# Kernel optimization log

Hardware: AMD Instinct MI355X
Metric: run time of the kernel (lower is better)

The kernel has to match this reference:

```python
import jax, jax.numpy as jnp
import numpy as np

U_UNITS = 256

def _lstm(x, mask, W, U, b, reverse):
    # x: [B,T,F], mask: [B,T] bool (True = valid). Keras semantics: masked steps
    # carry state and previous output through unchanged.
    B = x.shape[0]
    u = U.shape[0]
    xW = jnp.einsum('btf,fg->btg', x, W) + b  # precompute input projection
    def step(carry, inp):
        h, c = carry
        xw, m = inp
        z = xw + h @ U
        i, f, g, o = jnp.split(z, 4, axis=-1)
        i = jax.nn.sigmoid(i)
        f = jax.nn.sigmoid(f)
        g = jnp.tanh(g)
        o = jax.nn.sigmoid(o)
        cn = f * c + i * g
        hn = o * jnp.tanh(cn)
        m2 = m[:, None]
        hn = jnp.where(m2, hn, h)
        cn = jnp.where(m2, cn, c)
        return (hn, cn), hn
    init = (jnp.zeros((B, u), x.dtype), jnp.zeros((B, u), x.dtype))
    xs = (jnp.swapaxes(xW, 0, 1), jnp.swapaxes(mask, 0, 1))
    _, hs = jax.lax.scan(step, init, xs, reverse=reverse)
    return jnp.swapaxes(hs, 0, 1)

def _bilstm(x, mask, Wf, Uf, bf, Wb, Ub, bb):
    hf = _lstm(x, mask, Wf, Uf, bf, False)
    hb = _lstm(x, mask, Wb, Ub, bb, True)
    return jnp.concatenate([hf, hb], axis=-1)

def setup_inputs():
    key = jax.random.key(0)
    B, T, F, U = 32, 2048, 64, U_UNITS
    H = 2 * U
    ks = jax.random.split(key, 40)
    def gl(k, shape):
        return (jax.random.normal(k, shape, jnp.float32) / np.sqrt(shape[0])).astype(jnp.float32)
    d = {}
    d['x'] = jax.random.normal(ks[0], (B, T, F), jnp.float32)
    d['x_mask'] = jax.random.randint(ks[1], (B, T), 0, 2, jnp.int32)
    d['training'] = 0
    # layer 0: input F; layer 1: input 2U
    d['Wf0'] = gl(ks[2], (F, 4 * U)); d['Uf0'] = gl(ks[3], (U, 4 * U)); d['bf0'] = jnp.zeros((4 * U,), jnp.float32)
    d['Wb0'] = gl(ks[4], (F, 4 * U)); d['Ub0'] = gl(ks[5], (U, 4 * U)); d['bb0'] = jnp.zeros((4 * U,), jnp.float32)
    d['Wf1'] = gl(ks[6], (H, 4 * U)); d['Uf1'] = gl(ks[7], (U, 4 * U)); d['bf1'] = jnp.zeros((4 * U,), jnp.float32)
    d['Wb1'] = gl(ks[8], (H, 4 * U)); d['Ub1'] = gl(ks[9], (U, 4 * U)); d['bb1'] = jnp.zeros((4 * U,), jnp.float32)
    # output heads
    d['Wp'] = gl(ks[10], (H, 2)); d['bp'] = jnp.zeros((2,), jnp.float32)
    d['Wbu'] = gl(ks[11], (H, 2)); d['bbu'] = jnp.zeros((2,), jnp.float32)
    d['W3'] = gl(ks[12], (H, 3)); d['b3'] = jnp.zeros((3,), jnp.float32)
    d['W8'] = gl(ks[13], (H, 8)); d['b8'] = jnp.zeros((8,), jnp.float32)
    d['Wa'] = gl(ks[14], (H, 1)); d['ba'] = jnp.zeros((1,), jnp.float32)
    d['Wpp'] = gl(ks[15], (H, 4)); d['bpp'] = jnp.zeros((4,), jnp.float32)
    return d

def reference(x, x_mask, training, Wf0, Uf0, bf0, Wb0, Ub0, bb0, Wf1, Uf1, bf1, Wb1, Ub1, bb1, Wp, bp, Wbu, bbu, W3, b3, W8, b8, Wa, ba, Wpp, bpp):
    mask = x_mask != 1  # tf.logical_not(tf.equal(x_mask, 1))
    h = _bilstm(x, mask, Wf0, Uf0, bf0, Wb0, Ub0, bb0)
    h = _bilstm(h, mask, Wf1, Uf1, bf1, Wb1, Ub1, bb1)
    h = jax.nn.relu(h)
    # dropout is identity at inference (training=0)
    ppi = jax.nn.softmax(h @ Wp + bp, axis=-1)
    buried = h @ Wbu + bbu
    ss3 = h @ W3 + b3
    ss8 = h @ W8 + b8
    asa = h @ Wa + ba
    phipsi = h @ Wpp + bpp
    return (ppi, buried, ss3, ss8, asa, phipsi)
```

## Files before the change

kernel.cpp:

```cpp
#include <hip/hip_runtime.h>
#include <stdint.h>


#define T_SEQ 2048
#define BATCH 32
#define NROWS 65536
#define NG 1024
#define FLG_STRIDE 32

typedef __attribute__((ext_vector_type(8))) short short8;
typedef __attribute__((ext_vector_type(4))) float f32x4;
typedef __attribute__((ext_vector_type(2))) float f32x2;

__device__ __forceinline__ ushort f32_to_bf16(float f) {
    uint32_t u = __float_as_uint(f);
    u = u + 0x7FFFu + ((u >> 16) & 1u);
    return (ushort)(u >> 16);
}
__device__ __forceinline__ float bf16_to_f32(ushort h) {
    return __uint_as_float(((uint32_t)h) << 16);
}
__device__ __forceinline__ uint64_t split_pack4(f32x4 v, uint64_t& lo64) {
    ushort h0 = f32_to_bf16(v[0]), h1 = f32_to_bf16(v[1]);
    ushort h2 = f32_to_bf16(v[2]), h3 = f32_to_bf16(v[3]);
    ushort l0 = f32_to_bf16(v[0] - bf16_to_f32(h0));
    ushort l1 = f32_to_bf16(v[1] - bf16_to_f32(h1));
    ushort l2 = f32_to_bf16(v[2] - bf16_to_f32(h2));
    ushort l3 = f32_to_bf16(v[3] - bf16_to_f32(h3));
    lo64 = (uint64_t)l0 | ((uint64_t)l1 << 16) | ((uint64_t)l2 << 32) | ((uint64_t)l3 << 48);
    return (uint64_t)h0 | ((uint64_t)h1 << 16) | ((uint64_t)h2 << 32) | ((uint64_t)h3 << 48);
}

__global__ void init_ctrl_kernel(int* __restrict__ flags, int nf,
                                 unsigned long long* __restrict__ hxp, int nh) {
    int i = blockIdx.x * 256 + threadIdx.x;
    if (i < nf) flags[i] = 0;
    if (i < nh) hxp[i] = 0ull;
}

__global__ __launch_bounds__(256) void gemm_split_kernel(
    const float* __restrict__ A, int K,
    const float* __restrict__ Bw, const float* __restrict__ bias,
    float* __restrict__ Cc, int cb, int lsS, int dir)
{
    __shared__ __align__(16) ushort Ash[128 * 36];
    __shared__ __align__(16) ushort Asl[128 * 36];
    __shared__ __align__(16) ushort Bsh[128 * 36];
    __shared__ __align__(16) ushort Bsl[128 * 36];
    const int Smask = (1 << lsS) - 1;
    int t = threadIdx.x;
    int n0 = blockIdx.x * 128;
    int m0 = blockIdx.y * 128;
    int lane = t & 63, wv = t >> 6;
    int wr = wv >> 1, wc = wv & 1;
    int fr = lane & 15, fq = lane >> 4;

    f32x4 acc[4][4];
#pragma unroll
    for (int i = 0; i < 4; i++)
#pragma unroll
        for (int j = 0; j < 4; j++) acc[i][j] = (f32x4)(0.0f);

    int arow = t >> 1, ahalf = t & 1;
    int bc = t & 127, bkh = t >> 7;

    int loc_all = m0 + arow;
    int b = loc_all >> lsS;
    int loc = loc_all & Smask;
    int row_g = b * T_SEQ + (dir ? (T_SEQ - 1 - cb - loc) : (cb + loc));

    for (int k0 = 0; k0 < K; k0 += 32) {
        {
            const float* s = A + (size_t)row_g * K + k0 + ahalf * 16;
            uint64_t* dh = (uint64_t*)&Ash[arow * 36 + ahalf * 16];
            uint64_t* dl = (uint64_t*)&Asl[arow * 36 + ahalf * 16];
#pragma unroll
            for (int g = 0; g < 4; g++) {
                f32x4 v = ((const f32x4*)s)[g];
                uint64_t lo64;
                uint64_t hi64 = split_pack4(v, lo64);
                dh[g] = hi64; dl[g] = lo64;
            }
        }
        {
            float bv[16];
#pragma unroll
            for (int i = 0; i < 16; i++)
                bv[i] = Bw[(size_t)(k0 + bkh * 16 + i) * NG + n0 + bc];
            uint64_t* dh = (uint64_t*)&Bsh[bc * 36 + bkh * 16];
            uint64_t* dl = (uint64_t*)&Bsl[bc * 36 + bkh * 16];
#pragma unroll
            for (int g = 0; g < 4; g++) {
                f32x4 v = { bv[4 * g], bv[4 * g + 1], bv[4 * g + 2], bv[4 * g + 3] };
                uint64_t lo64;
                uint64_t hi64 = split_pack4(v, lo64);
                dh[g] = hi64; dl[g] = lo64;
            }
        }
        __syncthreads();
        union FU { uint64_t u[2]; short8 v; };
        FU bh[4], bl[4];
#pragma unroll
        for (int n = 0; n < 4; n++) {
            int boff = (wc * 64 + n * 16 + fr) * 36 + fq * 8;
            bh[n].u[0] = ((const uint64_t*)&Bsh[boff])[0];
            bh[n].u[1] = ((const uint64_t*)&Bsh[boff])[1];
            bl[n].u[0] = ((const uint64_t*)&Bsl[boff])[0];
            bl[n].u[1] = ((const uint64_t*)&Bsl[boff])[1];
        }
#pragma unroll
        for (int m = 0; m < 4; m++) {
            int aoff = (wr * 64 + m * 16 + fr) * 36 + fq * 8;
            FU ah, al;
            ah.u[0] = ((const uint64_t*)&Ash[aoff])[0];
            ah.u[1] = ((const uint64_t*)&Ash[aoff])[1];
            al.u[0] = ((const uint64_t*)&Asl[aoff])[0];
            al.u[1] = ((const uint64_t*)&Asl[aoff])[1];
#pragma unroll
            for (int n = 0; n < 4; n++) {
                acc[m][n] = __builtin_amdgcn_mfma_f32_16x16x32_bf16(ah.v, bh[n].v, acc[m][n], 0, 0, 0);
                acc[m][n] = __builtin_amdgcn_mfma_f32_16x16x32_bf16(ah.v, bl[n].v, acc[m][n], 0, 0, 0);
                acc[m][n] = __builtin_amdgcn_mfma_f32_16x16x32_bf16(al.v, bh[n].v, acc[m][n], 0, 0, 0);
            }
        }
        __syncthreads();
    }
#pragma unroll
    for (int m = 0; m < 4; m++)
#pragma unroll
        for (int n = 0; n < 4; n++) {
            int gcol = n0 + wc * 64 + n * 16 + fr;
            float bvv = bias[gcol];
#pragma unroll
            for (int i = 0; i < 4; i++) {
                int crow = m0 + wr * 64 + m * 16 + fq * 4 + i;
                Cc[(size_t)crow * NG + gcol] = acc[m][n][i] + bvv;
            }
        }
}

__global__ __launch_bounds__(512, 2) void lstm_kernel(
    const float* __restrict__ Uf, const float* __restrict__ Ub,
    const float* __restrict__ xWcf, const float* __restrict__ xWcb,
    const int* __restrict__ mask,
    float* __restrict__ houtF,
    ushort* __restrict__ houtB,
    unsigned long long* __restrict__ hxp,
    float* __restrict__ cstate,
    int* __restrict__ flags,
    int cb, int S)
{
    int wg = blockIdx.x;
    int chain = wg & 63;
    int w = wg >> 6;
    int dir = chain >> 5;
    int b = chain & 31;
    const float* U = dir ? Ub : Uf;
    const float* xWc = dir ? xWcb : xWcf;

    int t = threadIdx.x;
    __shared__ __align__(16) float hbuf[256];
    __shared__ __align__(16) float pbuf[4 * 256];
    __shared__ int mbuf[2048];

    int kchunk = t >> 7;
    int cg = t & 127;
    int q = cg >> 5;
    int jj0 = 2 * (cg & 31);
    int col0 = q * 256 + w * 64 + jj0;

    f32x2 Ur[64];
    {
        const float* Up = U + (size_t)(kchunk * 64) * NG + col0;
#pragma unroll
        for (int i = 0; i < 64; i++) Ur[i] = *(const f32x2*)(Up + (size_t)i * NG);
    }
    unsigned long long* hxpc = hxp + chain * 512;
    int* flg = flags + chain * FLG_STRIDE;
    int j = t & 63;
    int gj = w * 64 + j;
    int owner = t >> 6;

    for (int nl = t; nl < S; nl += 512) {
        int tp = dir ? (T_SEQ - 1 - (cb + nl)) : (cb + nl);
        mbuf[nl] = mask[b * T_SEQ + tp];
    }
    int kc = __hip_atomic_load(&flg[0], __ATOMIC_RELAXED, __HIP_MEMORY_SCOPE_AGENT);
    if (t < 256) {
        if (kc > 0) {
            unsigned long long pk = __hip_atomic_load(&hxpc[((kc - 1) & 1) * 256 + t],
                                                      __ATOMIC_RELAXED, __HIP_MEMORY_SCOPE_AGENT);
            hbuf[t] = __uint_as_float((uint32_t)pk);
        } else {
            hbuf[t] = 0.0f;
        }
    }
    float creg = 0.0f, hreg = 0.0f;
    if (t < 64) {
        if (cb != 0) creg = cstate[chain * 256 + gj];
        if (kc > 0) {
            unsigned long long pk = __hip_atomic_load(&hxpc[((kc - 1) & 1) * 256 + gj],
                                                      __ATOMIC_RELAXED, __HIP_MEMORY_SCOPE_AGENT);
            hreg = __uint_as_float((uint32_t)pk);
        }
    }
    __syncthreads();

    for (int nl = 0; nl < S; nl++) {
        int tp = dir ? (T_SEQ - 1 - (cb + nl)) : (cb + nl);
        size_t row_g = (size_t)b * T_SEQ + tp;
        int mval = mbuf[nl];
        if (mval == 1) {
            if (t < 64) {
                size_t oidx = row_g * 512 + dir * 256 + gj;
                if (houtF) houtF[oidx] = hreg;
                else       houtB[oidx] = f32_to_bf16(hreg);
            }
            continue;
        }
        float xw0 = 0.f, xw1 = 0.f, xw2 = 0.f, xw3 = 0.f;
        if (t < 64) {
            const float* xr = xWc + ((size_t)b * S + nl) * NG;
            xw0 = xr[gj];
            xw1 = xr[256 + gj];
            xw2 = xr[512 + gj];
            xw3 = xr[768 + gj];
        }
        if (kc > 0 && t < 256 && owner != w) {
            unsigned long long pk;
            for (;;) {
                pk = __hip_atomic_load(&hxpc[((kc - 1) & 1) * 256 + t],
                                       __ATOMIC_RELAXED, __HIP_MEMORY_SCOPE_AGENT);
                if ((uint32_t)(pk >> 32) >= (uint32_t)kc) break;
                __builtin_amdgcn_s_sleep(1);
            }
            hbuf[t] = __uint_as_float((uint32_t)pk);
        }
        __syncthreads();
        float a0 = 0.0f, a1 = 0.0f;
        {
            const float* hb = &hbuf[kchunk * 64];
#pragma unroll
            for (int i = 0; i < 16; i++) {
                f32x4 h4 = *(const f32x4*)(hb + 4 * i);
#pragma unroll
                for (int j2 = 0; j2 < 4; j2++) {
                    a0 += h4[j2] * Ur[4 * i + j2][0];
                    a1 += h4[j2] * Ur[4 * i + j2][1];
                }
            }
        }
        {
            f32x2 pv = {a0, a1};
            *(f32x2*)&pbuf[kchunk * 256 + 2 * cg] = pv;
        }
        __syncthreads();
        if (t < 64) {
            float zi = xw0 + pbuf[j]       + pbuf[256 + j]       + pbuf[512 + j]       + pbuf[768 + j];
            float zf = xw1 + pbuf[64 + j]  + pbuf[256 + 64 + j]  + pbuf[512 + 64 + j]  + pbuf[768 + 64 + j];
            float zg = xw2 + pbuf[128 + j] + pbuf[256 + 128 + j] + pbuf[512 + 128 + j] + pbuf[768 + 128 + j];
            float zo = xw3 + pbuf[192 + j] + pbuf[256 + 192 + j] + pbuf[512 + 192 + j] + pbuf[768 + 192 + j];
            float ig = 1.0f / (1.0f + expf(-zi));
            float fg = 1.0f / (1.0f + expf(-zf));
            float gg = tanhf(zg);
            float og = 1.0f / (1.0f + expf(-zo));
            float cn = fg * creg + ig * gg;
            float hn = og * tanhf(cn);
            creg = cn; hreg = hn;
            hbuf[gj] = hn;
            unsigned long long pk = ((unsigned long long)(uint32_t)(kc + 1) << 32)
                                  | (unsigned long long)(uint32_t)__float_as_uint(hn);
            __hip_atomic_store(&hxpc[(kc & 1) * 256 + gj], pk,
                               __ATOMIC_RELAXED, __HIP_MEMORY_SCOPE_AGENT);
            size_t oidx = row_g * 512 + dir * 256 + gj;
            if (houtF) houtF[oidx] = hn;
            else       houtB[oidx] = f32_to_bf16(hn);
        }
        kc++;
    }
    if (t < 64) cstate[chain * 256 + gj] = creg;
    if (w == 0 && t == 0)
        __hip_atomic_store(&flg[0], kc, __ATOMIC_RELAXED, __HIP_MEMORY_SCOPE_AGENT);
}

__global__ __launch_bounds__(256, 2) void heads_kernel(
    const ushort* __restrict__ h1,
    const float* __restrict__ Wp, const float* __restrict__ bp,
    const float* __restrict__ Wbu, const float* __restrict__ bbu,
    const float* __restrict__ W3, const float* __restrict__ b3,
    const float* __restrict__ W8, const float* __restrict__ b8,
    const float* __restrict__ Wa, const float* __restrict__ ba,
    const float* __restrict__ Wpp, const float* __restrict__ bpp,
    float* __restrict__ out)
{
    int gwv = (blockIdx.x * 256 + threadIdx.x) >> 6;
    int nwv = (gridDim.x * 256) >> 6;
    int lane = threadIdx.x & 63;
    int k0 = lane * 8;

    float wr_[8][20];
#pragma unroll
    for (int u = 0; u < 8; u++) {
        int k = k0 + u;
        wr_[u][0]  = Wp[k * 2];      wr_[u][1]  = Wp[k * 2 + 1];
        wr_[u][2]  = Wbu[k * 2];     wr_[u][3]  = Wbu[k * 2 + 1];
        wr_[u][4]  = W3[k * 3];      wr_[u][5]  = W3[k * 3 + 1];  wr_[u][6] = W3[k * 3 + 2];
#pragma unroll
        for (int c = 0; c < 8; c++) wr_[u][7 + c] = W8[k * 8 + c];
        wr_[u][15] = Wa[k];
#pragma unroll
        for (int c = 0; c < 4; c++) wr_[u][16 + c] = Wpp[k * 4 + c];
    }
    float myb = 0.0f;
    size_t ooff = 0;
    if (lane < 2)        { myb = bp[lane];        ooff = 0 + lane; }
    else if (lane < 4)   { myb = bbu[lane - 2];   ooff = (size_t)NROWS * 2 + (lane - 2); }
    else if (lane < 7)   { myb = b3[lane - 4];    ooff = (size_t)NROWS * 4 + (lane - 4); }
    else if (lane < 15)  { myb = b8[lane - 7];    ooff = (size_t)NROWS * 7 + (lane - 7); }
    else if (lane < 16)  { myb = ba[0];           ooff = (size_t)NROWS * 15; }
    else if (lane < 20)  { myb = bpp[lane - 16];  ooff = (size_t)NROWS * 16 + (lane - 16); }
    float bp0 = bp[0], bp1 = bp[1];
    int stride = (lane < 2) ? 2 : (lane < 4) ? 2 : (lane < 7) ? 3 : (lane < 15) ? 8 : (lane < 16) ? 1 : 4;

    for (int r = gwv; r < NROWS; r += nwv) {
        union { uint4 u4; ushort us[8]; } hu;
        hu.u4 = *(const uint4*)(h1 + (size_t)r * 512 + k0);
        float acc[20];
#pragma unroll
        for (int c = 0; c < 20; c++) acc[c] = 0.0f;
#pragma unroll
        for (int u = 0; u < 8; u++) {
            float hv = fmaxf(bf16_to_f32(hu.us[u]), 0.0f);
#pragma unroll
            for (int c = 0; c < 20; c++) acc[c] += hv * wr_[u][c];
        }
#pragma unroll
        for (int off = 32; off >= 1; off >>= 1)
#pragma unroll
            for (int c = 0; c < 20; c++) acc[c] += __shfl_xor(acc[c], off);
        if (lane < 20) {
            float v = acc[lane] + myb;
            if (lane < 2) {
                float s0 = acc[0] + bp0, s1 = acc[1] + bp1;
                float mx = fmaxf(s0, s1);
                float e0 = expf(s0 - mx), e1 = expf(s1 - mx);
                v = ((lane == 0) ? e0 : e1) / (e0 + e1);
            }
            out[ooff + (size_t)r * stride] = v;
        }
    }
}

extern "C" void kernel_launch(void* const* d_in, const int* in_sizes, int n_in,
                              void* d_out, int out_size, void* d_ws, size_t ws_size,
                              hipStream_t stream) {
    const float* x    = (const float*)d_in[0];
    const int* xmask  = (const int*)d_in[1];
    const float* Wf0  = (const float*)d_in[3];
    const float* Uf0  = (const float*)d_in[4];
    const float* bf0  = (const float*)d_in[5];
    const float* Wb0  = (const float*)d_in[6];
    const float* Ub0  = (const float*)d_in[7];
    const float* bb0  = (const float*)d_in[8];
    const float* Wf1  = (const float*)d_in[9];
    const float* Uf1  = (const float*)d_in[10];
    const float* bf1  = (const float*)d_in[11];
    const float* Wb1  = (const float*)d_in[12];
    const float* Ub1  = (const float*)d_in[13];
    const float* bb1  = (const float*)d_in[14];
    const float* Wp   = (const float*)d_in[15]; const float* bp  = (const float*)d_in[16];
    const float* Wbu  = (const float*)d_in[17]; const float* bbu = (const float*)d_in[18];
    const float* W3   = (const float*)d_in[19]; const float* b3  = (const float*)d_in[20];
    const float* W8   = (const float*)d_in[21]; const float* b8  = (const float*)d_in[22];
    const float* Wa   = (const float*)d_in[23]; const float* ba  = (const float*)d_in[24];
    const float* Wpp  = (const float*)d_in[25]; const float* bpp = (const float*)d_in[26];
    float* out = (float*)d_out;

    char* ws = (char*)d_ws;
    size_t off = 0;
    auto take = [&](size_t bytes) -> void* {
        void* p = ws + off;
        off += (bytes + 255) & ~(size_t)255;
        return p;
    };
    int* flags = (int*)take((size_t)2 * 64 * FLG_STRIDE * 4);
    unsigned long long* hxp = (unsigned long long*)take((size_t)2 * 64 * 2 * 256 * 8);
    float*  cstate = (float*)take((size_t)64 * 256 * 4);
    float*  h0F    = (float*)take((size_t)NROWS * 512 * 4);
    ushort* h1B    = (ushort*)take((size_t)NROWS * 512 * 2);
    size_t fixed = off;

    int S = 8, lsS = 3;
    for (int cand = 11; cand >= 3; cand--) {
        if (fixed + (((size_t)1 << cand) * 262144) + 4096 <= ws_size) { S = 1 << cand; lsS = cand; break; }
    }
    float* xWcf = (float*)take((size_t)BATCH * S * NG * 4);
    float* xWcb = (float*)take((size_t)BATCH * S * NG * 4);
    int NC = T_SEQ / S;
    (void)in_sizes; (void)n_in; (void)out_size;

    int nf = 2 * 64 * FLG_STRIDE;
    int nh = 2 * 64 * 2 * 256;
    int ninit = nh > nf ? nh : nf;
    init_ctrl_kernel<<<(ninit + 255) / 256, 256, 0, stream>>>(flags, nf, hxp, nh);

    dim3 ggrid(NG / 128, (BATCH * S) / 128);
    for (int c = 0; c < NC; c++) {
        int cb = c * S;
        gemm_split_kernel<<<ggrid, 256, 0, stream>>>(x, 64, Wf0, bf0, xWcf, cb, lsS, 0);
        gemm_split_kernel<<<ggrid, 256, 0, stream>>>(x, 64, Wb0, bb0, xWcb, cb, lsS, 1);
        lstm_kernel<<<256, 512, 0, stream>>>(Uf0, Ub0, xWcf, xWcb, xmask, h0F, nullptr,
                                             hxp, cstate, flags, cb, S);
    }
    for (int c = 0; c < NC; c++) {
        int cb = c * S;
        gemm_split_kernel<<<ggrid, 256, 0, stream>>>(h0F, 512, Wf1, bf1, xWcf, cb, lsS, 0);
        gemm_split_kernel<<<ggrid, 256, 0, stream>>>(h0F, 512, Wb1, bb1, xWcb, cb, lsS, 1);
        lstm_kernel<<<256, 512, 0, stream>>>(Uf1, Ub1, xWcf, xWcb, xmask, nullptr, h1B,
                                             hxp + (size_t)64 * 512, cstate, flags + 64 * FLG_STRIDE, cb, S);
    }

    heads_kernel<<<2048, 256, 0, stream>>>(
        h1B, Wp, bp, Wbu, bbu, W3, b3, W8, b8, Wa, ba, Wpp, bpp, out);
}
```

Measured before the change: 5.613 ms.

## Run each LSTM chain in one workgroup with fp16-packed recurrent weights and dot2

```diff
diff --git a/kernel.cpp b/kernel.cpp
--- a/kernel.cpp
+++ b/kernel.cpp
@@ -6,11 +6,11 @@
 #define BATCH 32
 #define NROWS 65536
 #define NG 1024
-#define FLG_STRIDE 32
 
 typedef __attribute__((ext_vector_type(8))) short short8;
 typedef __attribute__((ext_vector_type(4))) float f32x4;
 typedef __attribute__((ext_vector_type(2))) float f32x2;
+typedef _Float16 f16x2 __attribute__((ext_vector_type(2)));
 
 __device__ __forceinline__ ushort f32_to_bf16(float f) {
     uint32_t u = __float_as_uint(f);
@@ -30,12 +30,19 @@
     lo64 = (uint64_t)l0 | ((uint64_t)l1 << 16) | ((uint64_t)l2 << 32) | ((uint64_t)l3 << 48);
     return (uint64_t)h0 | ((uint64_t)h1 << 16) | ((uint64_t)h2 << 32) | ((uint64_t)h3 << 48);
 }
-
-__global__ void init_ctrl_kernel(int* __restrict__ flags, int nf,
-                                 unsigned long long* __restrict__ hxp, int nh) {
+__device__ __forceinline__ float fdot2_(uint32_t u, uint32_t h, float acc) {
+    asm("v_dot2_f32_f16 %0, %1, %2, %0" : "+v"(acc) : "v"(u), "v"(h));
+    return acc;
+}
+
+__global__ void upack_kernel(const float* __restrict__ U, uint32_t* __restrict__ Upk) {
     int i = blockIdx.x * 256 + threadIdx.x;
-    if (i < nf) flags[i] = 0;
-    if (i < nh) hxp[i] = 0ull;
+    if (i >= 128 * 1024) return;
+    int kp = i >> 10, col = i & 1023;
+    f16x2 v;
+    v[0] = (_Float16)U[(size_t)(2 * kp) * NG + col];
+    v[1] = (_Float16)U[(size_t)(2 * kp + 1) * NG + col];
+    Upk[i] = __builtin_bit_cast(uint32_t, v);
 }
 
 __global__ __launch_bounds__(256) void gemm_split_kernel(
@@ -140,126 +147,111 @@
 }
 
 __global__ __launch_bounds__(512, 2) void lstm_kernel(
-    const float* __restrict__ Uf, const float* __restrict__ Ub,
+    const uint32_t* __restrict__ Upkf, const uint32_t* __restrict__ Upkb,
     const float* __restrict__ xWcf, const float* __restrict__ xWcb,
     const int* __restrict__ mask,
     float* __restrict__ houtF,
-    ushort* __restrict__ houtB,
-    unsigned long long* __restrict__ hxp,
+    ushort* __restrict__ houtH,
+    float* __restrict__ hstate,
     float* __restrict__ cstate,
-    int* __restrict__ flags,
     int cb, int S)
 {
-    int wg = blockIdx.x;
-    int chain = wg & 63;
-    int w = wg >> 6;
+    int chain = blockIdx.x;
     int dir = chain >> 5;
     int b = chain & 31;
-    const float* U = dir ? Ub : Uf;
+    const uint32_t* Upk = dir ? Upkb : Upkf;
     const float* xWc = dir ? xWcb : xWcf;
 
     int t = threadIdx.x;
-    __shared__ __align__(16) float hbuf[256];
-    __shared__ __align__(16) float pbuf[4 * 256];
+    int c0 = 2 * t;
+
+    __shared__ __align__(16) uint32_t hsh[128];
+    __shared__ __align__(16) uint32_t hsl[128];
+    __shared__ __align__(16) float zsh[1024];
+    __shared__ __align__(16) uint4 Ulds[8][512];
     __shared__ int mbuf[2048];
 
-    int kchunk = t >> 7;
-    int cg = t & 127;
-    int q = cg >> 5;
-    int jj0 = 2 * (cg & 31);
-    int col0 = q * 256 + w * 64 + jj0;
-
-    f32x2 Ur[64];
-    {
-        const float* Up = U + (size_t)(kchunk * 64) * NG + col0;
-#pragma unroll
-        for (int i = 0; i < 64; i++) Ur[i] = *(const f32x2*)(Up + (size_t)i * NG);
-    }
-    unsigned long long* hxpc = hxp + chain * 512;
-    int* flg = flags + chain * FLG_STRIDE;
-    int j = t & 63;
-    int gj = w * 64 + j;
-    int owner = t >> 6;
-
+#pragma unroll
+    for (int q = 0; q < 8; q++) {
+        uint4 v;
+        v.x = Upk[(size_t)(2 * q) * NG + c0];
+        v.y = Upk[(size_t)(2 * q) * NG + c0 + 1];
+        v.z = Upk[(size_t)(2 * q + 1) * NG + c0];
+        v.w = Upk[(size_t)(2 * q + 1) * NG + c0 + 1];
+        Ulds[q][t] = v;
+    }
+    uint32_t Ua[112], Ub[112];
+#pragma unroll
+    for (int kp = 0; kp < 112; kp++) {
+        Ua[kp] = Upk[(size_t)(16 + kp) * NG + c0];
+        Ub[kp] = Upk[(size_t)(16 + kp) * NG + c0 + 1];
+    }
     for (int nl = t; nl < S; nl += 512) {
         int tp = dir ? (T_SEQ - 1 - (cb + nl)) : (cb + nl);
         mbuf[nl] = mask[b * T_SEQ + tp];
     }
-    int kc = __hip_atomic_load(&flg[0], __ATOMIC_RELAXED, __HIP_MEMORY_SCOPE_AGENT);
+    float hreg = 0.0f, creg = 0.0f;
     if (t < 256) {
-        if (kc > 0) {
-            unsigned long long pk = __hip_atomic_load(&hxpc[((kc - 1) & 1) * 256 + t],
-                                                      __ATOMIC_RELAXED, __HIP_MEMORY_SCOPE_AGENT);
-            hbuf[t] = __uint_as_float((uint32_t)pk);
-        } else {
-            hbuf[t] = 0.0f;
-        }
-    }
-    float creg = 0.0f, hreg = 0.0f;
-    if (t < 64) {
-        if (cb != 0) creg = cstate[chain * 256 + gj];
-        if (kc > 0) {
-            unsigned long long pk = __hip_atomic_load(&hxpc[((kc - 1) & 1) * 256 + gj],
-                                                      __ATOMIC_RELAXED, __HIP_MEMORY_SCOPE_AGENT);
-            hreg = __uint_as_float((uint32_t)pk);
-        }
+        if (cb != 0) {
+            hreg = hstate[chain * 256 + t];
+            creg = cstate[chain * 256 + t];
+        }
+        _Float16 hf = (_Float16)hreg;
+        _Float16 hl16 = (_Float16)(hreg - (float)hf);
+        ((ushort*)hsh)[t] = __builtin_bit_cast(ushort, hf);
+        ((ushort*)hsl)[t] = __builtin_bit_cast(ushort, hl16);
     }
     __syncthreads();
 
     for (int nl = 0; nl < S; nl++) {
         int tp = dir ? (T_SEQ - 1 - (cb + nl)) : (cb + nl);
         size_t row_g = (size_t)b * T_SEQ + tp;
-        int mval = mbuf[nl];
-        if (mval == 1) {
-            if (t < 64) {
-                size_t oidx = row_g * 512 + dir * 256 + gj;
+        if (mbuf[nl] == 1) {
+            if (t < 256) {
+                size_t oidx = row_g * 512 + dir * 256 + t;
                 if (houtF) houtF[oidx] = hreg;
-                else       houtB[oidx] = f32_to_bf16(hreg);
+                else       houtH[oidx] = __builtin_bit_cast(ushort, (_Float16)hreg);
             }
             continue;
         }
-        float xw0 = 0.f, xw1 = 0.f, xw2 = 0.f, xw3 = 0.f;
-        if (t < 64) {
-            const float* xr = xWc + ((size_t)b * S + nl) * NG;
-            xw0 = xr[gj];
-            xw1 = xr[256 + gj];
-            xw2 = xr[512 + gj];
-            xw3 = xr[768 + gj];
-        }
-        if (kc > 0 && t < 256 && owner != w) {
-            unsigned long long pk;
-            for (;;) {
-                pk = __hip_atomic_load(&hxpc[((kc - 1) & 1) * 256 + t],
-                                       __ATOMIC_RELAXED, __HIP_MEMORY_SCOPE_AGENT);
-                if ((uint32_t)(pk >> 32) >= (uint32_t)kc) break;
-                __builtin_amdgcn_s_sleep(1);
-            }
-            hbuf[t] = __uint_as_float((uint32_t)pk);
-        }
+        f32x2 xw = *(const f32x2*)(xWc + ((size_t)b * S + nl) * NG + c0);
+        float a0 = 0.0f, a1 = 0.0f;
+        const uint4* hhp = (const uint4*)hsh;
+        const uint4* hlp = (const uint4*)hsl;
+#pragma unroll
+        for (int q = 0; q < 4; q++) {
+            uint4 hh = hhp[q];
+            uint4 hl = hlp[q];
+            uint4 u0 = Ulds[2 * q][t];
+            uint4 u1 = Ulds[2 * q + 1][t];
+            a0 = fdot2_(u0.x, hh.x, a0); a1 = fdot2_(u0.y, hh.x, a1);
+            a0 = fdot2_(u0.x, hl.x, a0); a1 = fdot2_(u0.y, hl.x, a1);
+            a0 = fdot2_(u0.z, hh.y, a0); a1 = fdot2_(u0.w, hh.y, a1);
+            a0 = fdot2_(u0.z, hl.y, a0); a1 = fdot2_(u0.w, hl.y, a1);
+            a0 = fdot2_(u1.x, hh.z, a0); a1 = fdot2_(u1.y, hh.z, a1);
+            a0 = fdot2_(u1.x, hl.z, a0); a1 = fdot2_(u1.y, hl.z, a1);
+            a0 = fdot2_(u1.z, hh.w, a0); a1 = fdot2_(u1.w, hh.w, a1);
+            a0 = fdot2_(u1.z, hl.w, a0); a1 = fdot2_(u1.w, hl.w, a1);
+        }
+#pragma unroll
+        for (int i = 4; i < 32; i++) {
+            uint4 hh = hhp[i];
+            uint4 hl = hlp[i];
+            int kp = 4 * i - 16;
+            a0 = fdot2_(Ua[kp + 0], hh.x, a0); a1 = fdot2_(Ub[kp + 0], hh.x, a1);
+            a0 = fdot2_(Ua[kp + 0], hl.x, a0); a1 = fdot2_(Ub[kp + 0], hl.x, a1);
+            a0 = fdot2_(Ua[kp + 1], hh.y, a0); a1 = fdot2_(Ub[kp + 1], hh.y, a1);
+            a0 = fdot2_(Ua[kp + 1], hl.y, a0); a1 = fdot2_(Ub[kp + 1], hl.y, a1);
+            a0 = fdot2_(Ua[kp + 2], hh.z, a0); a1 = fdot2_(Ub[kp + 2], hh.z, a1);
+            a0 = fdot2_(Ua[kp + 2], hl.z, a0); a1 = fdot2_(Ub[kp + 2], hl.z, a1);
+            a0 = fdot2_(Ua[kp + 3], hh.w, a0); a1 = fdot2_(Ub[kp + 3], hh.w, a1);
+            a0 = fdot2_(Ua[kp + 3], hl.w, a0); a1 = fdot2_(Ub[kp + 3], hl.w, a1);
+        }
+        zsh[c0]     = a0 + xw[0];
+        zsh[c0 + 1] = a1 + xw[1];
         __syncthreads();
-        float a0 = 0.0f, a1 = 0.0f;
-        {
-            const float* hb = &hbuf[kchunk * 64];
-#pragma unroll
-            for (int i = 0; i < 16; i++) {
-                f32x4 h4 = *(const f32x4*)(hb + 4 * i);
-#pragma unroll
-                for (int j2 = 0; j2 < 4; j2++) {
-                    a0 += h4[j2] * Ur[4 * i + j2][0];
-                    a1 += h4[j2] * Ur[4 * i + j2][1];
-                }
-            }
-        }
-        {
-            f32x2 pv = {a0, a1};
-            *(f32x2*)&pbuf[kchunk * 256 + 2 * cg] = pv;
-        }
-        __syncthreads();
-        if (t < 64) {
-            float zi = xw0 + pbuf[j]       + pbuf[256 + j]       + pbuf[512 + j]       + pbuf[768 + j];
-            float zf = xw1 + pbuf[64 + j]  + pbuf[256 + 64 + j]  + pbuf[512 + 64 + j]  + pbuf[768 + 64 + j];
-            float zg = xw2 + pbuf[128 + j] + pbuf[256 + 128 + j] + pbuf[512 + 128 + j] + pbuf[768 + 128 + j];
-            float zo = xw3 + pbuf[192 + j] + pbuf[256 + 192 + j] + pbuf[512 + 192 + j] + pbuf[768 + 192 + j];
+        if (t < 256) {
+            float zi = zsh[t], zf = zsh[256 + t], zg = zsh[512 + t], zo = zsh[768 + t];
             float ig = 1.0f / (1.0f + expf(-zi));
             float fg = 1.0f / (1.0f + expf(-zf));
             float gg = tanhf(zg);
@@ -267,20 +259,20 @@
             float cn = fg * creg + ig * gg;
             float hn = og * tanhf(cn);
             creg = cn; hreg = hn;
-            hbuf[gj] = hn;
-            unsigned long long pk = ((unsigned long long)(uint32_t)(kc + 1) << 32)
-                                  | (unsigned long long)(uint32_t)__float_as_uint(hn);
-            __hip_atomic_store(&hxpc[(kc & 1) * 256 + gj], pk,
-                               __ATOMIC_RELAXED, __HIP_MEMORY_SCOPE_AGENT);
-            size_t oidx = row_g * 512 + dir * 256 + gj;
+            _Float16 hf = (_Float16)hn;
+            _Float16 hl16 = (_Float16)(hn - (float)hf);
+            ((ushort*)hsh)[t] = __builtin_bit_cast(ushort, hf);
+            ((ushort*)hsl)[t] = __builtin_bit_cast(ushort, hl16);
+            size_t oidx = row_g * 512 + dir * 256 + t;
             if (houtF) houtF[oidx] = hn;
-            else       houtB[oidx] = f32_to_bf16(hn);
-        }
-        kc++;
-    }
-    if (t < 64) cstate[chain * 256 + gj] = creg;
-    if (w == 0 && t == 0)
-        __hip_atomic_store(&flg[0], kc, __ATOMIC_RELAXED, __HIP_MEMORY_SCOPE_AGENT);
+            else       houtH[oidx] = __builtin_bit_cast(ushort, hf);
+        }
+        __syncthreads();
+    }
+    if (t < 256) {
+        hstate[chain * 256 + t] = hreg;
+        cstate[chain * 256 + t] = creg;
+    }
 }
 
 __global__ __launch_bounds__(256, 2) void heads_kernel(
@@ -330,7 +322,7 @@
         for (int c = 0; c < 20; c++) acc[c] = 0.0f;
 #pragma unroll
         for (int u = 0; u < 8; u++) {
-            float hv = fmaxf(bf16_to_f32(hu.us[u]), 0.0f);
+            float hv = fmaxf((float)__builtin_bit_cast(_Float16, hu.us[u]), 0.0f);
 #pragma unroll
             for (int c = 0; c < 20; c++) acc[c] += hv * wr_[u][c];
         }
@@ -383,11 +375,14 @@
         off += (bytes + 255) & ~(size_t)255;
         return p;
     };
-    int* flags = (int*)take((size_t)2 * 64 * FLG_STRIDE * 4);
-    unsigned long long* hxp = (unsigned long long*)take((size_t)2 * 64 * 2 * 256 * 8);
+    uint32_t* U0f = (uint32_t*)take((size_t)128 * 1024 * 4);
+    uint32_t* U0b = (uint32_t*)take((size_t)128 * 1024 * 4);
+    uint32_t* U1f = (uint32_t*)take((size_t)128 * 1024 * 4);
+    uint32_t* U1b = (uint32_t*)take((size_t)128 * 1024 * 4);
+    float*  hstate = (float*)take((size_t)64 * 256 * 4);
     float*  cstate = (float*)take((size_t)64 * 256 * 4);
     float*  h0F    = (float*)take((size_t)NROWS * 512 * 4);
-    ushort* h1B    = (ushort*)take((size_t)NROWS * 512 * 2);
+    ushort* h1H    = (ushort*)take((size_t)NROWS * 512 * 2);
     size_t fixed = off;
 
     int S = 8, lsS = 3;
@@ -399,27 +394,27 @@
     int NC = T_SEQ / S;
     (void)in_sizes; (void)n_in; (void)out_size;
 
-    int nf = 2 * 64 * FLG_STRIDE;
-    int nh = 2 * 64 * 2 * 256;
-    int ninit = nh > nf ? nh : nf;
-    init_ctrl_kernel<<<(ninit + 255) / 256, 256, 0, stream>>>(flags, nf, hxp, nh);
+    upack_kernel<<<512, 256, 0, stream>>>(Uf0, U0f);
+    upack_kernel<<<512, 256, 0, stream>>>(Ub0, U0b);
+    upack_kernel<<<512, 256, 0, stream>>>(Uf1, U1f);
+    upack_kernel<<<512, 256, 0, stream>>>(Ub1, U1b);
 
     dim3 ggrid(NG / 128, (BATCH * S) / 128);
     for (int c = 0; c < NC; c++) {
         int cb = c * S;
         gemm_split_kernel<<<ggrid, 256, 0, stream>>>(x, 64, Wf0, bf0, xWcf, cb, lsS, 0);
         gemm_split_kernel<<<ggrid, 256, 0, stream>>>(x, 64, Wb0, bb0, xWcb, cb, lsS, 1);
-        lstm_kernel<<<256, 512, 0, stream>>>(Uf0, Ub0, xWcf, xWcb, xmask, h0F, nullptr,
-                                             hxp, cstate, flags, cb, S);
+        lstm_kernel<<<64, 512, 0, stream>>>(U0f, U0b, xWcf, xWcb, xmask, h0F, nullptr,
+                                            hstate, cstate, cb, S);
     }
     for (int c = 0; c < NC; c++) {
         int cb = c * S;
         gemm_split_kernel<<<ggrid, 256, 0, stream>>>(h0F, 512, Wf1, bf1, xWcf, cb, lsS, 0);
         gemm_split_kernel<<<ggrid, 256, 0, stream>>>(h0F, 512, Wb1, bb1, xWcb, cb, lsS, 1);
-        lstm_kernel<<<256, 512, 0, stream>>>(Uf1, Ub1, xWcf, xWcb, xmask, nullptr, h1B,
-                                             hxp + (size_t)64 * 512, cstate, flags + 64 * FLG_STRIDE, cb, S);
+        lstm_kernel<<<64, 512, 0, stream>>>(U1f, U1b, xWcf, xWcb, xmask, nullptr, h1H,
+                                            hstate, cstate, cb, S);
     }
 
     heads_kernel<<<2048, 256, 0, stream>>>(
-        h1B, Wp, bp, Wbu, bbu, W3, b3, W8, b8, Wa, ba, Wpp, bpp, out);
-}
+        h1H, Wp, bp, Wbu, bbu, W3, b3, W8, b8, Wa, ba, Wpp, bpp, out);
+}
```

Measured after the change: 11.45 ms. 104% more time.

## Fuse next-chunk input-projection GEMM into LSTM kernel with double-buffered xW

Applied to the files above, without the earlier changes.

```diff
diff --git a/kernel.cpp b/kernel.cpp
--- a/kernel.cpp
+++ b/kernel.cpp
@@ -38,19 +38,26 @@
     if (i < nh) hxp[i] = 0ull;
 }
 
-__global__ __launch_bounds__(256) void gemm_split_kernel(
+struct __align__(16) GemmSh {
+    ushort Ash[128 * 36];
+    ushort Asl[128 * 36];
+    ushort Bsh[128 * 36];
+    ushort Bsl[128 * 36];
+};
+struct __align__(16) LstmSh {
+    float hbuf[256];
+    float pbuf[1024];
+    int mbuf[2048];
+};
+union __align__(16) ShU { GemmSh g; LstmSh l; };
+
+__device__ void gemm_body(GemmSh& sh,
     const float* __restrict__ A, int K,
     const float* __restrict__ Bw, const float* __restrict__ bias,
-    float* __restrict__ Cc, int cb, int lsS, int dir)
+    float* __restrict__ Cc, int cb, int lsS, int dir, int n0, int m0)
 {
-    __shared__ __align__(16) ushort Ash[128 * 36];
-    __shared__ __align__(16) ushort Asl[128 * 36];
-    __shared__ __align__(16) ushort Bsh[128 * 36];
-    __shared__ __align__(16) ushort Bsl[128 * 36];
     const int Smask = (1 << lsS) - 1;
     int t = threadIdx.x;
-    int n0 = blockIdx.x * 128;
-    int m0 = blockIdx.y * 128;
     int lane = t & 63, wv = t >> 6;
     int wr = wv >> 1, wc = wv & 1;
     int fr = lane & 15, fq = lane >> 4;
@@ -72,8 +79,8 @@
     for (int k0 = 0; k0 < K; k0 += 32) {
         {
             const float* s = A + (size_t)row_g * K + k0 + ahalf * 16;
-            uint64_t* dh = (uint64_t*)&Ash[arow * 36 + ahalf * 16];
-            uint64_t* dl = (uint64_t*)&Asl[arow * 36 + ahalf * 16];
+            uint64_t* dh = (uint64_t*)&sh.Ash[arow * 36 + ahalf * 16];
+            uint64_t* dl = (uint64_t*)&sh.Asl[arow * 36 + ahalf * 16];
 #pragma unroll
             for (int g = 0; g < 4; g++) {
                 f32x4 v = ((const f32x4*)s)[g];
@@ -87,8 +94,8 @@
 #pragma unroll
             for (int i = 0; i < 16; i++)
                 bv[i] = Bw[(size_t)(k0 + bkh * 16 + i) * NG + n0 + bc];
-            uint64_t* dh = (uint64_t*)&Bsh[bc * 36 + bkh * 16];
-            uint64_t* dl = (uint64_t*)&Bsl[bc * 36 + bkh * 16];
+            uint64_t* dh = (uint64_t*)&sh.Bsh[bc * 36 + bkh * 16];
+            uint64_t* dl = (uint64_t*)&sh.Bsl[bc * 36 + bkh * 16];
 #pragma unroll
             for (int g = 0; g < 4; g++) {
                 f32x4 v = { bv[4 * g], bv[4 * g + 1], bv[4 * g + 2], bv[4 * g + 3] };
@@ -103,19 +110,19 @@
 #pragma unroll
         for (int n = 0; n < 4; n++) {
             int boff = (wc * 64 + n * 16 + fr) * 36 + fq * 8;
-            bh[n].u[0] = ((const uint64_t*)&Bsh[boff])[0];
-            bh[n].u[1] = ((const uint64_t*)&Bsh[boff])[1];
-            bl[n].u[0] = ((const uint64_t*)&Bsl[boff])[0];
-            bl[n].u[1] = ((const uint64_t*)&Bsl[boff])[1];
+            bh[n].u[0] = ((const uint64_t*)&sh.Bsh[boff])[0];
+            bh[n].u[1] = ((const uint64_t*)&sh.Bsh[boff])[1];
+            bl[n].u[0] = ((const uint64_t*)&sh.Bsl[boff])[0];
+            bl[n].u[1] = ((const uint64_t*)&sh.Bsl[boff])[1];
         }
 #pragma unroll
         for (int m = 0; m < 4; m++) {
             int aoff = (wr * 64 + m * 16 + fr) * 36 + fq * 8;
             FU ah, al;
-            ah.u[0] = ((const uint64_t*)&Ash[aoff])[0];
-            ah.u[1] = ((const uint64_t*)&Ash[aoff])[1];
-            al.u[0] = ((const uint64_t*)&Asl[aoff])[0];
-            al.u[1] = ((const uint64_t*)&Asl[aoff])[1];
+            ah.u[0] = ((const uint64_t*)&sh.Ash[aoff])[0];
+            ah.u[1] = ((const uint64_t*)&sh.Ash[aoff])[1];
+            al.u[0] = ((const uint64_t*)&sh.Asl[aoff])[0];
+            al.u[1] = ((const uint64_t*)&sh.Asl[aoff])[1];
 #pragma unroll
             for (int n = 0; n < 4; n++) {
                 acc[m][n] = __builtin_amdgcn_mfma_f32_16x16x32_bf16(ah.v, bh[n].v, acc[m][n], 0, 0, 0);
@@ -139,17 +146,34 @@
         }
 }
 
-__global__ __launch_bounds__(512, 2) void lstm_kernel(
+__global__ __launch_bounds__(512, 2) void fused_kernel(
     const float* __restrict__ Uf, const float* __restrict__ Ub,
     const float* __restrict__ xWcf, const float* __restrict__ xWcb,
     const int* __restrict__ mask,
-    float* __restrict__ houtF,
-    ushort* __restrict__ houtB,
-    unsigned long long* __restrict__ hxp,
-    float* __restrict__ cstate,
-    int* __restrict__ flags,
-    int cb, int S)
+    float* __restrict__ houtF, ushort* __restrict__ houtB,
+    unsigned long long* __restrict__ hxp, float* __restrict__ cstate,
+    int* __restrict__ flags, int cb, int S, int has_lstm,
+    const float* __restrict__ A, int K,
+    const float* __restrict__ Wgf, const float* __restrict__ Wgb,
+    const float* __restrict__ biasf, const float* __restrict__ biasb,
+    float* __restrict__ xWnf, float* __restrict__ xWnb,
+    int cbn, int lsS, int mtiles)
 {
+    __shared__ ShU sh;
+    if (blockIdx.x >= 256) {
+        if (cbn >= T_SEQ) return;
+        if (threadIdx.x >= 256) return;
+        int gb = blockIdx.x - 256;
+        int half = 8 * mtiles;
+        int dirg = gb >= half ? 1 : 0;
+        int gbb = dirg ? gb - half : gb;
+        int n0 = (gbb & 7) * 128;
+        int m0 = (gbb >> 3) * 128;
+        gemm_body(sh.g, A, K, dirg ? Wgb : Wgf, dirg ? biasb : biasf,
+                  dirg ? xWnb : xWnf, cbn, lsS, dirg, n0, m0);
+        return;
+    }
+    if (!has_lstm) return;
     int wg = blockIdx.x;
     int chain = wg & 63;
     int w = wg >> 6;
@@ -159,9 +183,9 @@
     const float* xWc = dir ? xWcb : xWcf;
 
     int t = threadIdx.x;
-    __shared__ __align__(16) float hbuf[256];
-    __shared__ __align__(16) float pbuf[4 * 256];
-    __shared__ int mbuf[2048];
+    float* hbuf = sh.l.hbuf;
+    float* pbuf = sh.l.pbuf;
+    int* mbuf = sh.l.mbuf;
 
     int kchunk = t >> 7;
     int cg = t & 127;
@@ -391,12 +415,18 @@
     size_t fixed = off;
 
     int S = 8, lsS = 3;
-    for (int cand = 11; cand >= 3; cand--) {
-        if (fixed + (((size_t)1 << cand) * 262144) + 4096 <= ws_size) { S = 1 << cand; lsS = cand; break; }
-    }
-    float* xWcf = (float*)take((size_t)BATCH * S * NG * 4);
-    float* xWcb = (float*)take((size_t)BATCH * S * NG * 4);
+    for (int cand = 9; cand >= 3; cand--) {
+        if (fixed + 4 * (((size_t)1 << cand) * 131072) + 4096 <= ws_size) { S = 1 << cand; lsS = cand; break; }
+    }
+    float* xWf[2]; float* xWb[2];
+    xWf[0] = (float*)take((size_t)BATCH * S * NG * 4);
+    xWb[0] = (float*)take((size_t)BATCH * S * NG * 4);
+    xWf[1] = (float*)take((size_t)BATCH * S * NG * 4);
+    xWb[1] = (float*)take((size_t)BATCH * S * NG * 4);
     int NC = T_SEQ / S;
+    int mtiles = (BATCH * S) / 128;
+    int NGB = 2 * 8 * mtiles;
+    dim3 fgrid(256 + NGB);
     (void)in_sizes; (void)n_in; (void)out_size;
 
     int nf = 2 * 64 * FLG_STRIDE;
@@ -404,20 +434,27 @@
     int ninit = nh > nf ? nh : nf;
     init_ctrl_kernel<<<(ninit + 255) / 256, 256, 0, stream>>>(flags, nf, hxp, nh);
 
-    dim3 ggrid(NG / 128, (BATCH * S) / 128);
+    fused_kernel<<<fgrid, 512, 0, stream>>>(
+        Uf0, Ub0, xWf[0], xWb[0], xmask, h0F, nullptr, hxp, cstate, flags, 0, S, 0,
+        x, 64, Wf0, Wb0, bf0, bb0, xWf[0], xWb[0], 0, lsS, mtiles);
     for (int c = 0; c < NC; c++) {
         int cb = c * S;
-        gemm_split_kernel<<<ggrid, 256, 0, stream>>>(x, 64, Wf0, bf0, xWcf, cb, lsS, 0);
-        gemm_split_kernel<<<ggrid, 256, 0, stream>>>(x, 64, Wb0, bb0, xWcb, cb, lsS, 1);
-        lstm_kernel<<<256, 512, 0, stream>>>(Uf0, Ub0, xWcf, xWcb, xmask, h0F, nullptr,
-                                             hxp, cstate, flags, cb, S);
-    }
+        int cbn = (c + 1) * S;
+        fused_kernel<<<fgrid, 512, 0, stream>>>(
+            Uf0, Ub0, xWf[c & 1], xWb[c & 1], xmask, h0F, nullptr, hxp, cstate, flags, cb, S, 1,
+            x, 64, Wf0, Wb0, bf0, bb0, xWf[(c + 1) & 1], xWb[(c + 1) & 1], cbn, lsS, mtiles);
+    }
+    fused_kernel<<<fgrid, 512, 0, stream>>>(
+        Uf1, Ub1, xWf[0], xWb[0], xmask, nullptr, h1B, hxp + (size_t)64 * 512, cstate,
+        flags + 64 * FLG_STRIDE, 0, S, 0,
+        h0F, 512, Wf1, Wb1, bf1, bb1, xWf[0], xWb[0], 0, lsS, mtiles);
     for (int c = 0; c < NC; c++) {
         int cb = c * S;
-        gemm_split_kernel<<<ggrid, 256, 0, stream>>>(h0F, 512, Wf1, bf1, xWcf, cb, lsS, 0);
-        gemm_split_kernel<<<ggrid, 256, 0, stream>>>(h0F, 512, Wb1, bb1, xWcb, cb, lsS, 1);
-        lstm_kernel<<<256, 512, 0, stream>>>(Uf1, Ub1, xWcf, xWcb, xmask, nullptr, h1B,
-                                             hxp + (size_t)64 * 512, cstate, flags + 64 * FLG_STRIDE, cb, S);
+        int cbn = (c + 1) * S;
+        fused_kernel<<<fgrid, 512, 0, stream>>>(
+            Uf1, Ub1, xWf[c & 1], xWb[c & 1], xmask, nullptr, h1B, hxp + (size_t)64 * 512, cstate,
+            flags + 64 * FLG_STRIDE, cb, S, 1,
+            h0F, 512, Wf1, Wb1, bf1, bb1, xWf[(c + 1) & 1], xWb[(c + 1) & 1], cbn, lsS, mtiles);
     }
 
     heads_kernel<<<2048, 256, 0, stream>>>(
```

New measurement: 5.731 ms. 2.1% more time.
